# Performance work log

Hardware: AMD Instinct MI355X
Metric: run time of the kernel (lower is better)

Reference implementation:

```python
import jax, jax.numpy as jnp
import numpy as np

NUM_EMBEDDINGS = 1024
EMBEDDING_DIM = 512
B, H, W = 32, 32, 32


def setup_inputs() -> dict:
    key = jax.random.key(0)
    k1, k2 = jax.random.split(key)
    z = jax.random.normal(k1, (B, EMBEDDING_DIM, H, W), dtype=jnp.float32)
    embedding = jax.random.normal(k2, (NUM_EMBEDDINGS, EMBEDDING_DIM), dtype=jnp.float32)
    return {"z": z, "embedding": embedding}


def reference(z, embedding):
    # z: [B, C, H, W] -> [B, H, W, C] -> [N, C]
    zp = jnp.transpose(z, (0, 2, 3, 1))
    b, h, w, d = zp.shape
    z_flat = zp.reshape(-1, d)
    # squared L2 distances: ||z||^2 - 2 z e^T + ||e||^2  -> [N, K]
    distances = (
        jnp.sum(z_flat ** 2, axis=1, keepdims=True)
        - 2.0 * (z_flat @ embedding.T)
        + jnp.sum(embedding ** 2, axis=1)
    )
    indices = jnp.argmin(distances, axis=1)  # [N]
    # one-hot @ embedding == direct gather
    quantized = embedding[indices]  # [N, d]
    quantized = quantized.reshape(b, h, w, d).transpose(0, 3, 1, 2)  # [B, C, H, W]
    return quantized, 0.0, indices.reshape(b, -1)
```

## Files before the change

### kernel.cpp

```cpp
#include <hip/hip_runtime.h>
#include <cfloat>

typedef _Float16 half8 __attribute__((ext_vector_type(8)));
typedef float    f32x4 __attribute__((ext_vector_type(4)));
typedef unsigned int  uint;
typedef unsigned short ushort;

constexpr int DIM  = 512;
constexpr int NEMB = 1024;
constexpr int HW   = 1024;
constexpr int NROW = 32 * HW;

constexpr long long QCOUNT = (long long)32 * 512 * 32 * 32;
constexpr long long SOFF   = QCOUNT;
constexpr long long IOFF   = SOFF + 1;

constexpr size_t WS_ZT    = 0;
constexpr size_t WS_ET    = 33554432;
constexpr size_t WS_ENORM = 34603008;
constexpr size_t WS_CNT   = 34607104;
constexpr size_t WS_LIST  = 34607360;
constexpr size_t WS_CANDB = WS_LIST + (size_t)NROW * 4;
constexpr size_t WS_CANDI = WS_CANDB + (size_t)2 * NROW * 8;
constexpr size_t WS_NEED  = WS_CANDI + (size_t)2 * NROW * 4;

constexpr float DELTA = 0.25f;

__device__ __forceinline__ void gld16(const void* g, void* l) {
    __builtin_amdgcn_global_load_lds(
        (const __attribute__((address_space(1))) void*)g,
        (__attribute__((address_space(3))) void*)l, 16, 0, 0);
}
union PKH8 { half8 v; _Float16 h[8]; };

__device__ __forceinline__ int swz_slot(int r, int g) {
    return g ^ ((r >> 1) & 3);
}

__global__ __launch_bounds__(256) void eprep(const float* __restrict__ e,
                                             char* __restrict__ et,
                                             float* __restrict__ enorm,
                                             int* __restrict__ cnt) {
    if (blockIdx.x == 0 && threadIdx.x == 0) *cnt = 0;
    int gid = blockIdx.x * 256 + threadIdx.x;
    int ke  = gid >> 6;
    int kbg = gid & 63;
    const float* src = e + (size_t)ke * DIM + kbg * 8;
    PKH8 h;
    float s = 0.f;
    #pragma unroll
    for (int j = 0; j < 8; ++j) {
        float v = src[j];
        h.h[j] = (_Float16)v;
        s += v * v;
    }
    int nc = ke >> 7, r = ke & 127, kc = kbg >> 2, g = kbg & 3;
    size_t byte = ((size_t)(nc * 16 + kc)) * 8192 + (size_t)r * 64
                + ((size_t)swz_slot(r, g) << 4);
    *reinterpret_cast<half8*>(et + byte) = h.v;
    #pragma unroll
    for (int off = 32; off > 0; off >>= 1) s += __shfl_down(s, off, 64);
    if (kbg == 0) enorm[ke] = s;
}

__global__ __launch_bounds__(256) void zprep(const float* __restrict__ z,
                                             char* __restrict__ zt) {
    __shared__ float ls[64][65];
    const int bx = blockIdx.x;
    const int mb = bx >> 3, kcc = bx & 7;
    const int n0 = mb * 64;
    const int b  = n0 >> 10;
    const int hw0 = n0 & (HW - 1);
    const int t = threadIdx.x;
    const int c4 = t >> 6, lane = t & 63;
    #pragma unroll
    for (int rnd = 0; rnd < 16; ++rnd) {
        int cl = c4 + rnd * 4;
        ls[cl][lane] = z[((size_t)(b * DIM + kcc * 64 + cl)) * HW + hw0 + lane];
    }
    __syncthreads();
    for (int g = t; g < 512; g += 256) {
        int r = g >> 3, kbl = g & 7;
        PKH8 h;
        #pragma unroll
        for (int jj = 0; jj < 8; ++jj) h.h[jj] = (_Float16)ls[kbl * 8 + jj][r];
        int kc_l = kbl >> 2, gg = kbl & 3;
        size_t tile = (size_t)mb * 16 + kcc * 2 + kc_l;
        size_t byte = tile * 4096 + (size_t)r * 64 + ((size_t)swz_slot(r, gg) << 4);
        *reinterpret_cast<half8*>(zt + byte) = h.v;
    }
}

#define VQ_STAGE(SS)                                                           \
  {                                                                            \
    const int kc_ = (SS) & 15;                                                 \
    const size_t tB_ = ((size_t)((half * 4 + ((SS) >> 4)) * 16 + kc_)) * 8192; \
    char* dst_ = smem + ((SS) % 3) * 12288;                                    \
    gld16(zt + zbase + (size_t)kc_ * 4096 + toff, dst_ + toff);                \
    gld16(et + tB_ + toff,        dst_ + 4096 + toff);                         \
    gld16(et + tB_ + 4096 + toff, dst_ + 8192 + toff);                         \
  }

#define VQ_STEP(S, VMLIT)                                                      \
  {                                                                            \
    asm volatile("s_waitcnt vmcnt(" VMLIT ")" ::: "memory");                   \
    __builtin_amdgcn_s_barrier();                                              \
    const char* buf_ = smem + ((S) % 3) * 12288;                               \
    half8 ah0 = *reinterpret_cast<const half8*>(buf_ + aoff0);                 \
    half8 ah1 = *reinterpret_cast<const half8*>(buf_ + aoff1);                 \
    half8 bh0 = *reinterpret_cast<const half8*>(buf_ + 4096 + boff0);          \
    half8 bh1 = *reinterpret_cast<const half8*>(buf_ + 4096 + boff1);          \
    half8 bh2 = *reinterpret_cast<const half8*>(buf_ + 4096 + boff2);          \
    half8 bh3 = *reinterpret_cast<const half8*>(buf_ + 4096 + boff3);          \
    asm volatile("s_waitcnt lgkmcnt(0)" ::: "memory");                         \
    __builtin_amdgcn_sched_barrier(0);                                         \
    __builtin_amdgcn_s_barrier();                                              \
    if ((S) + 3 < 64) VQ_STAGE((S) + 3);                                       \
    acc[0][0] = __builtin_amdgcn_mfma_f32_16x16x32_f16(ah0, bh0, acc[0][0], 0, 0, 0); \
    acc[0][1] = __builtin_amdgcn_mfma_f32_16x16x32_f16(ah0, bh1, acc[0][1], 0, 0, 0); \
    acc[0][2] = __builtin_amdgcn_mfma_f32_16x16x32_f16(ah0, bh2, acc[0][2], 0, 0, 0); \
    acc[0][3] = __builtin_amdgcn_mfma_f32_16x16x32_f16(ah0, bh3, acc[0][3], 0, 0, 0); \
    acc[1][0] = __builtin_amdgcn_mfma_f32_16x16x32_f16(ah1, bh0, acc[1][0], 0, 0, 0); \
    acc[1][1] = __builtin_amdgcn_mfma_f32_16x16x32_f16(ah1, bh1, acc[1][1], 0, 0, 0); \
    acc[1][2] = __builtin_amdgcn_mfma_f32_16x16x32_f16(ah1, bh2, acc[1][2], 0, 0, 0); \
    acc[1][3] = __builtin_amdgcn_mfma_f32_16x16x32_f16(ah1, bh3, acc[1][3], 0, 0, 0); \
    if (((S) & 15) == 15) {                                                    \
      const int ncl_ = ((S) >> 4) * 128;                                       \
      _Pragma("unroll")                                                        \
      for (int n = 0; n < 4; ++n) {                                            \
        const int lcol = ncl_ + wc * 64 + n * 16 + lr;                         \
        const float en = enorm_l[lcol];                                        \
        const int col = half * 512 + lcol;                                     \
        _Pragma("unroll")                                                      \
        for (int m = 0; m < 2; ++m) {                                          \
          _Pragma("unroll")                                                    \
          for (int q = 0; q < 4; ++q) {                                        \
            float dv = en - 2.0f * acc[m][n][q];                               \
            int sl = m * 4 + q;                                                \
            if (dv < b1v[sl]) { b2v[sl] = b1v[sl]; b1v[sl] = dv; i1v[sl] = col; } \
            else if (dv < b2v[sl]) b2v[sl] = dv;                               \
          }                                                                    \
        }                                                                      \
      }                                                                        \
      _Pragma("unroll")                                                        \
      for (int m = 0; m < 2; ++m)                                              \
        _Pragma("unroll")                                                      \
        for (int n = 0; n < 4; ++n) acc[m][n] = (f32x4)(0.f);                  \
    }                                                                          \
  }

__global__ __launch_bounds__(256, 4) void vq_mfma(const char* __restrict__ zt,
                                                  const char* __restrict__ et,
                                                  const float* __restrict__ enorm,
                                                  float2* __restrict__ cand_b,
                                                  int* __restrict__ cand_i) {
    __shared__ __align__(16) char smem[36864];
    __shared__ float enorm_l[512];

    const int t = threadIdx.x;
    const int w = t >> 6, l = t & 63;
    const int lr = l & 15, hg = l >> 4;
    const int wr = w >> 1;
    const int wc = w & 1;
    const int bid = blockIdx.x;
    const int mb = bid >> 1;
    const int half = bid & 1;
    const int n0 = mb * 64;

    const int swz = swz_slot(lr, hg) << 4;
    const int aoff0 = (wr * 32 + lr) * 64 + swz;
    const int aoff1 = (wr * 32 + 16 + lr) * 64 + swz;
    const int boff0 = (wc * 64 + lr) * 64 + swz;
    const int boff1 = (wc * 64 + 16 + lr) * 64 + swz;
    const int boff2 = (wc * 64 + 32 + lr) * 64 + swz;
    const int boff3 = (wc * 64 + 48 + lr) * 64 + swz;

    enorm_l[t]       = enorm[half * 512 + t];
    enorm_l[t + 256] = enorm[half * 512 + t + 256];
    __syncthreads();

    float b1v[8], b2v[8]; int i1v[8];
    #pragma unroll
    for (int s = 0; s < 8; ++s) { b1v[s] = FLT_MAX; b2v[s] = FLT_MAX; i1v[s] = 0; }

    const size_t zbase = (size_t)mb * 16 * 4096;
    const int toff = t * 16;

    f32x4 acc[2][4];
    #pragma unroll
    for (int m = 0; m < 2; ++m)
        #pragma unroll
        for (int n = 0; n < 4; ++n) acc[m][n] = (f32x4)(0.f);

    VQ_STAGE(0);
    VQ_STAGE(1);
    VQ_STAGE(2);

    for (int s = 0; s < 62; ++s) {
        VQ_STEP(s, "6");
    }
    VQ_STEP(62, "3");
    VQ_STEP(63, "0");

    #pragma unroll
    for (int s = 0; s < 8; ++s) {
        #pragma unroll
        for (int off = 1; off <= 8; off <<= 1) {
            float ob1 = __shfl_xor(b1v[s], off, 64);
            int   oi1 = __shfl_xor(i1v[s], off, 64);
            float ob2 = __shfl_xor(b2v[s], off, 64);
            if (ob1 < b1v[s] || (ob1 == b1v[s] && oi1 < i1v[s])) {
                b2v[s] = fminf(b1v[s], ob2);
                b1v[s] = ob1; i1v[s] = oi1;
            } else {
                b2v[s] = fminf(b2v[s], ob1);
            }
        }
    }
    __syncthreads();
    float* red_b1 = reinterpret_cast<float*>(smem);
    float* red_b2 = reinterpret_cast<float*>(smem + 512);
    int*   red_i1 = reinterpret_cast<int*>  (smem + 1024);
    if (lr == 0) {
        #pragma unroll
        for (int s = 0; s < 8; ++s) {
            int row = wr * 32 + (s >> 2) * 16 + hg * 4 + (s & 3);
            red_b1[row * 2 + wc] = b1v[s];
            red_b2[row * 2 + wc] = b2v[s];
            red_i1[row * 2 + wc] = i1v[s];
        }
    }
    __syncthreads();
    if (t < 64) {
        float a1 = red_b1[t * 2], a2 = red_b2[t * 2]; int ai = red_i1[t * 2];
        float c1 = red_b1[t * 2 + 1], c2 = red_b2[t * 2 + 1]; int ci = red_i1[t * 2 + 1];
        float B1, B2; int I1;
        if (c1 < a1 || (c1 == a1 && ci < ai)) { B1 = c1; I1 = ci; B2 = fminf(a1, c2); }
        else                                   { B1 = a1; I1 = ai; B2 = fminf(a2, c1); }
        cand_b[(size_t)half * NROW + n0 + t] = make_float2(B1, B2);
        cand_i[(size_t)half * NROW + n0 + t] = I1;
    }
}

__global__ __launch_bounds__(256) void combine(const float2* __restrict__ cand_b,
                                               const int* __restrict__ cand_i,
                                               const float* __restrict__ e,
                                               float* __restrict__ out,
                                               int* __restrict__ cnt,
                                               int* __restrict__ list) {
    __shared__ int idx_f[64];
    const int t = threadIdx.x;
    const int n0 = blockIdx.x * 64;
    if (t < 64) {
        const int row = n0 + t;
        float2 a = cand_b[row];
        float2 c = cand_b[NROW + row];
        int ai = cand_i[row];
        int ci = cand_i[NROW + row];
        float B1, B2; int I1;
        if (c.x < a.x) { B1 = c.x; I1 = ci; B2 = fminf(a.x, c.y); }
        else           { B1 = a.x; I1 = ai; B2 = fminf(a.y, c.x); }
        idx_f[t] = I1;
        out[IOFF + row] = (float)I1;
        if (B2 - B1 < DELTA) {
            int pos = atomicAdd(cnt, 1);
            list[pos] = row;
        }
    }
    if (blockIdx.x == 0 && t == 0) out[SOFF] = 0.0f;
    __syncthreads();

    const int b   = n0 >> 10;
    const int hw0 = n0 & (HW - 1);
    const int row4 = (t & 15) * 4;
    const int i0 = idx_f[row4 + 0];
    const int i1 = idx_f[row4 + 1];
    const int i2 = idx_f[row4 + 2];
    const int i3 = idx_f[row4 + 3];
    #pragma unroll 4
    for (int p = 0; p < 32; ++p) {
        int c = (t >> 4) + (p << 4);
        float4 v;
        v.x = e[(size_t)i0 * DIM + c];
        v.y = e[(size_t)i1 * DIM + c];
        v.z = e[(size_t)i2 * DIM + c];
        v.w = e[(size_t)i3 * DIM + c];
        *reinterpret_cast<float4*>(&out[((size_t)(b * DIM + c)) * HW + hw0 + row4]) = v;
    }
}

__global__ __launch_bounds__(256) void recheck(const float* __restrict__ z,
                                               const float* __restrict__ e,
                                               const float* __restrict__ enorm,
                                               const int* __restrict__ cnt,
                                               const int* __restrict__ list,
                                               float* __restrict__ out) {
    __shared__ float zrow[4][512];
    __shared__ float rb[256];
    __shared__ int   ri[256];
    __shared__ int   fidx[4];
    const int t = threadIdx.x;
    const int count = *cnt;
    const int ngrp = (count + 3) >> 2;
    for (int g = blockIdx.x; g < ngrp; g += gridDim.x) {
        const int base = g * 4;
        const int nr = min(4, count - base);
        __syncthreads();
        for (int r = 0; r < nr; ++r) {
            const int row = list[base + r];
            const int b = row >> 10, hw = row & (HW - 1);
            zrow[r][t]       = z[((size_t)(b * DIM + t))       * HW + hw];
            zrow[r][t + 256] = z[((size_t)(b * DIM + t + 256)) * HW + hw];
        }
        __syncthreads();
        float best[4]; int bi[4];
        #pragma unroll
        for (int r = 0; r < 4; ++r) { best[r] = FLT_MAX; bi[r] = 0; }
        #pragma unroll
        for (int p = 0; p < 4; ++p) {
            const int ke = t + p * 256;
            const float4* ep = reinterpret_cast<const float4*>(e + (size_t)ke * DIM);
            float d0 = 0.f, d1 = 0.f, d2 = 0.f, d3 = 0.f;
            const float4* z0 = reinterpret_cast<const float4*>(zrow[0]);
            const float4* z1 = reinterpret_cast<const float4*>(zrow[1]);
            const float4* z2 = reinterpret_cast<const float4*>(zrow[2]);
            const float4* z3 = reinterpret_cast<const float4*>(zrow[3]);
            for (int c = 0; c < 128; ++c) {
                float4 ev = ep[c];
                float4 a0 = z0[c], a1 = z1[c], a2 = z2[c], a3 = z3[c];
                d0 += ev.x*a0.x + ev.y*a0.y + ev.z*a0.z + ev.w*a0.w;
                d1 += ev.x*a1.x + ev.y*a1.y + ev.z*a1.z + ev.w*a1.w;
                d2 += ev.x*a2.x + ev.y*a2.y + ev.z*a2.z + ev.w*a2.w;
                d3 += ev.x*a3.x + ev.y*a3.y + ev.z*a3.z + ev.w*a3.w;
            }
            const float en = enorm[ke];
            float dd[4] = { en - 2.f*d0, en - 2.f*d1, en - 2.f*d2, en - 2.f*d3 };
            #pragma unroll
            for (int r = 0; r < 4; ++r)
                if (dd[r] < best[r]) { best[r] = dd[r]; bi[r] = ke; }
        }
        for (int r = 0; r < nr; ++r) {
            rb[t] = best[r]; ri[t] = bi[r];
            __syncthreads();
            #pragma unroll
            for (int s = 128; s > 0; s >>= 1) {
                if (t < s) {
                    float ov = rb[t + s]; int oi = ri[t + s];
                    if (ov < rb[t] || (ov == rb[t] && oi < ri[t])) {
                        rb[t] = ov; ri[t] = oi;
                    }
                }
                __syncthreads();
            }
            if (t == 0) {
                fidx[r] = ri[0];
                out[IOFF + list[base + r]] = (float)ri[0];
            }
            __syncthreads();
        }
        for (int r = 0; r < nr; ++r) {
            const int row = list[base + r];
            const int b = row >> 10, hw = row & (HW - 1);
            const int fbi = fidx[r];
            out[((size_t)(b * DIM + t))       * HW + hw] = e[(size_t)fbi * DIM + t];
            out[((size_t)(b * DIM + t + 256)) * HW + hw] = e[(size_t)fbi * DIM + t + 256];
        }
    }
}

constexpr int TM = 64;
constexpr int TN = 256;
constexpr int KC = 32;
constexpr int ZST = 68;
constexpr int EST = 260;

union F4 { float4 v; float f[4]; };

__global__ __launch_bounds__(256) void enorm_kernel(const float* __restrict__ e,
                                                    float* __restrict__ enorm) {
    int gid  = blockIdx.x * 256 + threadIdx.x;
    int wave = gid >> 6;
    int lane = gid & 63;
    if (wave >= NEMB) return;
    const float* row = e + (size_t)wave * DIM;
    float4 a = *reinterpret_cast<const float4*>(row + lane * 8);
    float4 b = *reinterpret_cast<const float4*>(row + lane * 8 + 4);
    float s = a.x*a.x + a.y*a.y + a.z*a.z + a.w*a.w
            + b.x*b.x + b.y*b.y + b.z*b.z + b.w*b.w;
    #pragma unroll
    for (int off = 32; off > 0; off >>= 1) s += __shfl_down(s, off, 64);
    if (lane == 0) enorm[wave] = s;
}

__global__ __launch_bounds__(256) void vq_main_kernel(const float* __restrict__ z,
                                                      const float* __restrict__ e,
                                                      const float* __restrict__ enorm,
                                                      float* __restrict__ out) {
    __shared__ float zs[KC][ZST];
    __shared__ float es[KC][EST];
    __shared__ float enorm_l[NEMB];
    __shared__ int   idx_f[TM];

    const int t   = threadIdx.x;
    const int n0  = blockIdx.x * TM;
    const int b   = n0 >> 10;
    const int hw0 = n0 & (HW - 1);
    const float* zb = z + ((size_t)b * DIM) * HW + hw0;

    #pragma unroll
    for (int i = 0; i < 4; ++i) enorm_l[t + i * 256] = enorm[t + i * 256];

    const int rg = t >> 5;
    const int cg = t & 31;

    float best[8];
    int   bidx[8];
    #pragma unroll
    for (int i = 0; i < 8; ++i) { best[i] = FLT_MAX; bidx[i] = 0; }

    const int z_r4 = (t & 15) * 4;
    const int z_c  = t >> 4;
    const int e_ke = t >> 3;
    const int e_c4 = t & 7;

    for (int nc = 0; nc < NEMB / TN; ++nc) {
        const int k0 = nc * TN;
        float acc[8][8];
        #pragma unroll
        for (int mi = 0; mi < 8; ++mi)
            #pragma unroll
            for (int nj = 0; nj < 8; ++nj) acc[mi][nj] = 0.f;

        for (int kc = 0; kc < DIM / KC; ++kc) {
            const int c0 = kc * KC;
            __syncthreads();
            #pragma unroll
            for (int p = 0; p < 2; ++p) {
                int c = z_c + p * 16;
                float4 v = *reinterpret_cast<const float4*>(zb + (size_t)(c0 + c) * HW + z_r4);
                *reinterpret_cast<float4*>(&zs[c][z_r4]) = v;
            }
            #pragma unroll
            for (int p = 0; p < 8; ++p) {
                int ke = e_ke + p * 32;
                float4 v = *reinterpret_cast<const float4*>(e + (size_t)(k0 + ke) * DIM + c0 + e_c4 * 4);
                es[e_c4 * 4 + 0][ke] = v.x;
                es[e_c4 * 4 + 1][ke] = v.y;
                es[e_c4 * 4 + 2][ke] = v.z;
                es[e_c4 * 4 + 3][ke] = v.w;
            }
            __syncthreads();
            #pragma unroll
            for (int kk = 0; kk < KC; ++kk) {
                F4 zf0, zf1, ef0, ef1;
                zf0.v = *reinterpret_cast<const float4*>(&zs[kk][rg * 8]);
                zf1.v = *reinterpret_cast<const float4*>(&zs[kk][rg * 8 + 4]);
                ef0.v = *reinterpret_cast<const float4*>(&es[kk][cg * 4]);
                ef1.v = *reinterpret_cast<const float4*>(&es[kk][128 + cg * 4]);
                #pragma unroll
                for (int mi = 0; mi < 4; ++mi) {
                    #pragma unroll
                    for (int nj = 0; nj < 4; ++nj) {
                        acc[mi][nj]         += zf0.f[mi] * ef0.f[nj];
                        acc[mi][nj + 4]     += zf0.f[mi] * ef1.f[nj];
                        acc[mi + 4][nj]     += zf1.f[mi] * ef0.f[nj];
                        acc[mi + 4][nj + 4] += zf1.f[mi] * ef1.f[nj];
                    }
                }
            }
        }
        #pragma unroll
        for (int mi = 0; mi < 8; ++mi) {
            #pragma unroll
            for (int nj = 0; nj < 8; ++nj) {
                int col = k0 + (nj < 4 ? cg * 4 + nj : 128 + cg * 4 + (nj - 4));
                float dv = enorm_l[col] - 2.0f * acc[mi][nj];
                if (dv < best[mi]) { best[mi] = dv; bidx[mi] = col; }
            }
        }
    }

    __syncthreads();
    float* best_l = reinterpret_cast<float*>(es);
    int*   idx_l  = reinterpret_cast<int*>(reinterpret_cast<char*>(es) + (size_t)TM * 33 * 4);
    #pragma unroll
    for (int mi = 0; mi < 8; ++mi) {
        int row = rg * 8 + mi;
        best_l[row * 33 + cg] = best[mi];
        idx_l[row * 33 + cg]  = bidx[mi];
    }
    __syncthreads();
    if (t < TM) {
        float bv = best_l[t * 33];
        int   bi = idx_l[t * 33];
        #pragma unroll
        for (int c = 1; c < 32; ++c) {
            float v  = best_l[t * 33 + c];
            int   ix = idx_l[t * 33 + c];
            if (v < bv || (v == bv && ix < bi)) { bv = v; bi = ix; }
        }
        idx_f[t] = bi;
        out[IOFF + n0 + t] = (float)bi;
    }
    if (blockIdx.x == 0 && t == 0) out[SOFF] = 0.0f;
    __syncthreads();

    const int row4 = (t & 15) * 4;
    const int i0 = idx_f[row4 + 0];
    const int i1 = idx_f[row4 + 1];
    const int i2 = idx_f[row4 + 2];
    const int i3 = idx_f[row4 + 3];
    #pragma unroll 4
    for (int p = 0; p < 32; ++p) {
        int c = (t >> 4) + (p << 4);
        float4 v;
        v.x = e[(size_t)i0 * DIM + c];
        v.y = e[(size_t)i1 * DIM + c];
        v.z = e[(size_t)i2 * DIM + c];
        v.w = e[(size_t)i3 * DIM + c];
        *reinterpret_cast<float4*>(&out[((size_t)(b * DIM + c)) * HW + hw0 + row4]) = v;
    }
}

extern "C" void kernel_launch(void* const* d_in, const int* in_sizes, int n_in,
                              void* d_out, int out_size, void* d_ws, size_t ws_size,
                              hipStream_t stream) {
    const float* z = (const float*)d_in[0];
    const float* e = (const float*)d_in[1];
    float* out = (float*)d_out;
    char*  ws  = (char*)d_ws;

    if (ws_size >= WS_NEED) {
        char*   zt     = ws + WS_ZT;
        char*   et     = ws + WS_ET;
        float*  enorm  = (float*)(ws + WS_ENORM);
        int*    cnt    = (int*)(ws + WS_CNT);
        int*    list   = (int*)(ws + WS_LIST);
        float2* cand_b = (float2*)(ws + WS_CANDB);
        int*    cand_i = (int*)(ws + WS_CANDI);

        hipLaunchKernelGGL(eprep,   dim3(256),           dim3(256), 0, stream, e, et, enorm, cnt);
        hipLaunchKernelGGL(zprep,   dim3(4096),          dim3(256), 0, stream, z, zt);
        hipLaunchKernelGGL(vq_mfma, dim3(NROW / 64 * 2), dim3(256), 0, stream,
                           zt, et, enorm, cand_b, cand_i);
        hipLaunchKernelGGL(combine, dim3(NROW / 64),     dim3(256), 0, stream,
                           cand_b, cand_i, e, out, cnt, list);
        hipLaunchKernelGGL(recheck, dim3(1024),          dim3(256), 0, stream,
                           z, e, enorm, cnt, list, out);
    } else {
        float* enorm = (float*)ws;
        hipLaunchKernelGGL(enorm_kernel,   dim3(NEMB / 4), dim3(256), 0, stream, e, enorm);
        hipLaunchKernelGGL(vq_main_kernel, dim3(NROW / TM), dim3(256), 0, stream,
                           z, e, enorm, out);
    }
}
```

Before: 213.5 us.

## Enlarge VQ MFMA tile to 128 rows with 512 threads and 4-stage pipeline

Doubles the row tile of the distance GEMM to 128 z-rows per block, with 512 threads (8 waves), so each loaded codebook tile is reused across twice as many rows. The z prep kernel is rewritten to emit 128-row tiles in the new layout. The LDS pipeline goes from 3 buffers to 4 with fixed buffer indices, and shared memory grows to 64KB plus the norm array. The larger LDS footprint and block size reduce how many blocks fit per CU, and the launch bound of 4 blocks of 512 threads may pressure registers.

```diff
diff --git a/kernel.cpp b/kernel.cpp
--- a/kernel.cpp
+++ b/kernel.cpp
@@ -65,57 +65,53 @@
 
 __global__ __launch_bounds__(256) void zprep(const float* __restrict__ z,
                                              char* __restrict__ zt) {
-    __shared__ float ls[64][65];
-    const int bx = blockIdx.x;
-    const int mb = bx >> 3, kcc = bx & 7;
-    const int n0 = mb * 64;
-    const int b  = n0 >> 10;
-    const int hw0 = n0 & (HW - 1);
+    __shared__ float ls[64][129];
+    const int bx  = blockIdx.x;
+    const int mb  = bx >> 3, kcc = bx & 7;
+    const int b   = mb >> 3;
+    const int hw0 = (mb & 7) * 128;
     const int t = threadIdx.x;
-    const int c4 = t >> 6, lane = t & 63;
-    #pragma unroll
-    for (int rnd = 0; rnd < 16; ++rnd) {
-        int cl = c4 + rnd * 4;
-        ls[cl][lane] = z[((size_t)(b * DIM + kcc * 64 + cl)) * HW + hw0 + lane];
-    }
-    __syncthreads();
-    for (int g = t; g < 512; g += 256) {
-        int r = g >> 3, kbl = g & 7;
+    for (int i = t; i < 64 * 128; i += 256) {
+        int c = i >> 7, hw = i & 127;
+        ls[c][hw] = z[((size_t)(b * DIM + kcc * 64 + c)) * HW + hw0 + hw];
+    }
+    __syncthreads();
+    for (int j = t; j < 1024; j += 256) {
+        int r = j >> 3, kbl = j & 7;
         PKH8 h;
         #pragma unroll
         for (int jj = 0; jj < 8; ++jj) h.h[jj] = (_Float16)ls[kbl * 8 + jj][r];
-        int kc_l = kbl >> 2, gg = kbl & 3;
-        size_t tile = (size_t)mb * 16 + kcc * 2 + kc_l;
-        size_t byte = tile * 4096 + (size_t)r * 64 + ((size_t)swz_slot(r, gg) << 4);
+        int kc = kcc * 2 + (kbl >> 2), g = kbl & 3;
+        size_t byte = ((size_t)(mb * 16 + kc)) * 8192 + (size_t)r * 64
+                    + ((size_t)swz_slot(r, g) << 4);
         *reinterpret_cast<half8*>(zt + byte) = h.v;
     }
 }
 
-#define VQ_STAGE(SS)                                                           \
+#define VQ_STAGE(SS, BUF)                                                      \
   {                                                                            \
     const int kc_ = (SS) & 15;                                                 \
-    const size_t tB_ = ((size_t)((half * 4 + ((SS) >> 4)) * 16 + kc_)) * 8192; \
-    char* dst_ = smem + ((SS) % 3) * 12288;                                    \
-    gld16(zt + zbase + (size_t)kc_ * 4096 + toff, dst_ + toff);                \
-    gld16(et + tB_ + toff,        dst_ + 4096 + toff);                         \
-    gld16(et + tB_ + 4096 + toff, dst_ + 8192 + toff);                         \
+    const size_t tB_ = ((size_t)((half4 + ((SS) >> 4)) * 16 + kc_)) * 8192;    \
+    char* dst_ = smem + (BUF) * 16384;                                         \
+    gld16(zt + zbase + (size_t)kc_ * 8192 + toff, dst_ + toff);                \
+    gld16(et + tB_ + toff, dst_ + 8192 + toff);                                \
   }
 
-#define VQ_STEP(S, VMLIT)                                                      \
+#define VQ_STEP(S, VMLIT, BUF)                                                 \
   {                                                                            \
     asm volatile("s_waitcnt vmcnt(" VMLIT ")" ::: "memory");                   \
     __builtin_amdgcn_s_barrier();                                              \
-    const char* buf_ = smem + ((S) % 3) * 12288;                               \
+    const char* buf_ = smem + (BUF) * 16384;                                   \
     half8 ah0 = *reinterpret_cast<const half8*>(buf_ + aoff0);                 \
     half8 ah1 = *reinterpret_cast<const half8*>(buf_ + aoff1);                 \
-    half8 bh0 = *reinterpret_cast<const half8*>(buf_ + 4096 + boff0);          \
-    half8 bh1 = *reinterpret_cast<const half8*>(buf_ + 4096 + boff1);          \
-    half8 bh2 = *reinterpret_cast<const half8*>(buf_ + 4096 + boff2);          \
-    half8 bh3 = *reinterpret_cast<const half8*>(buf_ + 4096 + boff3);          \
+    half8 bh0 = *reinterpret_cast<const half8*>(buf_ + 8192 + boff0);          \
+    half8 bh1 = *reinterpret_cast<const half8*>(buf_ + 8192 + boff1);          \
+    half8 bh2 = *reinterpret_cast<const half8*>(buf_ + 8192 + boff2);          \
+    half8 bh3 = *reinterpret_cast<const half8*>(buf_ + 8192 + boff3);          \
     asm volatile("s_waitcnt lgkmcnt(0)" ::: "memory");                         \
     __builtin_amdgcn_sched_barrier(0);                                         \
     __builtin_amdgcn_s_barrier();                                              \
-    if ((S) + 3 < 64) VQ_STAGE((S) + 3);                                       \
+    if ((S) + 4 < 64) VQ_STAGE((S) + 4, BUF);                                  \
     acc[0][0] = __builtin_amdgcn_mfma_f32_16x16x32_f16(ah0, bh0, acc[0][0], 0, 0, 0); \
     acc[0][1] = __builtin_amdgcn_mfma_f32_16x16x32_f16(ah0, bh1, acc[0][1], 0, 0, 0); \
     acc[0][2] = __builtin_amdgcn_mfma_f32_16x16x32_f16(ah0, bh2, acc[0][2], 0, 0, 0); \
@@ -149,12 +145,12 @@
     }                                                                          \
   }
 
-__global__ __launch_bounds__(256, 4) void vq_mfma(const char* __restrict__ zt,
+__global__ __launch_bounds__(512, 4) void vq_mfma(const char* __restrict__ zt,
                                                   const char* __restrict__ et,
                                                   const float* __restrict__ enorm,
                                                   float2* __restrict__ cand_b,
                                                   int* __restrict__ cand_i) {
-    __shared__ __align__(16) char smem[36864];
+    __shared__ __align__(16) char smem[65536];
     __shared__ float enorm_l[512];
 
     const int t = threadIdx.x;
@@ -165,7 +161,8 @@
     const int bid = blockIdx.x;
     const int mb = bid >> 1;
     const int half = bid & 1;
-    const int n0 = mb * 64;
+    const int half4 = half * 4;
+    const int n0 = mb * 128;
 
     const int swz = swz_slot(lr, hg) << 4;
     const int aoff0 = (wr * 32 + lr) * 64 + swz;
@@ -175,15 +172,14 @@
     const int boff2 = (wc * 64 + 32 + lr) * 64 + swz;
     const int boff3 = (wc * 64 + 48 + lr) * 64 + swz;
 
-    enorm_l[t]       = enorm[half * 512 + t];
-    enorm_l[t + 256] = enorm[half * 512 + t + 256];
+    enorm_l[t] = enorm[half * 512 + t];
     __syncthreads();
 
     float b1v[8], b2v[8]; int i1v[8];
     #pragma unroll
     for (int s = 0; s < 8; ++s) { b1v[s] = FLT_MAX; b2v[s] = FLT_MAX; i1v[s] = 0; }
 
-    const size_t zbase = (size_t)mb * 16 * 4096;
+    const size_t zbase = (size_t)mb * 16 * 8192;
     const int toff = t * 16;
 
     f32x4 acc[2][4];
@@ -192,15 +188,21 @@
         #pragma unroll
         for (int n = 0; n < 4; ++n) acc[m][n] = (f32x4)(0.f);
 
-    VQ_STAGE(0);
-    VQ_STAGE(1);
-    VQ_STAGE(2);
-
-    for (int s = 0; s < 62; ++s) {
-        VQ_STEP(s, "6");
-    }
-    VQ_STEP(62, "3");
-    VQ_STEP(63, "0");
+    VQ_STAGE(0, 0);
+    VQ_STAGE(1, 1);
+    VQ_STAGE(2, 2);
+    VQ_STAGE(3, 3);
+
+    for (int sp = 0; sp < 60; sp += 4) {
+        VQ_STEP(sp + 0, "6", 0);
+        VQ_STEP(sp + 1, "6", 1);
+        VQ_STEP(sp + 2, "6", 2);
+        VQ_STEP(sp + 3, "6", 3);
+    }
+    VQ_STEP(60, "6", 0);
+    VQ_STEP(61, "4", 1);
+    VQ_STEP(62, "2", 2);
+    VQ_STEP(63, "0", 3);
 
     #pragma unroll
     for (int s = 0; s < 8; ++s) {
@@ -219,8 +221,8 @@
     }
     __syncthreads();
     float* red_b1 = reinterpret_cast<float*>(smem);
-    float* red_b2 = reinterpret_cast<float*>(smem + 512);
-    int*   red_i1 = reinterpret_cast<int*>  (smem + 1024);
+    float* red_b2 = reinterpret_cast<float*>(smem + 1024);
+    int*   red_i1 = reinterpret_cast<int*>  (smem + 2048);
     if (lr == 0) {
         #pragma unroll
         for (int s = 0; s < 8; ++s) {
@@ -231,7 +233,7 @@
         }
     }
     __syncthreads();
-    if (t < 64) {
+    if (t < 128) {
         float a1 = red_b1[t * 2], a2 = red_b2[t * 2]; int ai = red_i1[t * 2];
         float c1 = red_b1[t * 2 + 1], c2 = red_b2[t * 2 + 1]; int ci = red_i1[t * 2 + 1];
         float B1, B2; int I1;
@@ -539,13 +541,13 @@
         float2* cand_b = (float2*)(ws + WS_CANDB);
         int*    cand_i = (int*)(ws + WS_CANDI);
 
-        hipLaunchKernelGGL(eprep,   dim3(256),           dim3(256), 0, stream, e, et, enorm, cnt);
-        hipLaunchKernelGGL(zprep,   dim3(4096),          dim3(256), 0, stream, z, zt);
-        hipLaunchKernelGGL(vq_mfma, dim3(NROW / 64 * 2), dim3(256), 0, stream,
+        hipLaunchKernelGGL(eprep,   dim3(256),            dim3(256), 0, stream, e, et, enorm, cnt);
+        hipLaunchKernelGGL(zprep,   dim3(2048),           dim3(256), 0, stream, z, zt);
+        hipLaunchKernelGGL(vq_mfma, dim3(NROW / 128 * 2), dim3(512), 0, stream,
                            zt, et, enorm, cand_b, cand_i);
-        hipLaunchKernelGGL(combine, dim3(NROW / 64),     dim3(256), 0, stream,
+        hipLaunchKernelGGL(combine, dim3(NROW / 64),      dim3(256), 0, stream,
                            cand_b, cand_i, e, out, cnt, list);
-        hipLaunchKernelGGL(recheck, dim3(1024),          dim3(256), 0, stream,
+        hipLaunchKernelGGL(recheck, dim3(1024),           dim3(256), 0, stream,
                            z, e, enorm, cnt, list, out);
     } else {
         float* enorm = (float*)ws;
```

New measurement: 219.8 us. 1.03x slower.
